# Kernel tuning notes

Measured on AMD Instinct MI355X. Metric: run time of the kernel, lower is better.

## Reference

```python
import jax, jax.numpy as jnp
import numpy as np

D_MODEL = 1024
NUM_HEADS = 16
D_K = D_MODEL // NUM_HEADS
BATCH = 4
SEQ = 2048


def setup_inputs() -> dict:
    key = jax.random.key(0)
    ks = jax.random.split(key, 12)
    s = 0.02
    inp = {
        "Q": jax.random.normal(ks[0], (BATCH, SEQ, D_MODEL), jnp.float32),
        "K": jax.random.normal(ks[1], (BATCH, SEQ, D_MODEL), jnp.float32),
        "V": jax.random.normal(ks[2], (BATCH, SEQ, D_MODEL), jnp.float32),
        "mask": jnp.tril(jnp.ones((SEQ, SEQ), jnp.int32)),  # causal: 0 = masked
        "Wq": jax.random.normal(ks[3], (D_MODEL, D_MODEL), jnp.float32) * s,
        "bq": jax.random.normal(ks[4], (D_MODEL,), jnp.float32) * s,
        "Wk": jax.random.normal(ks[5], (D_MODEL, D_MODEL), jnp.float32) * s,
        "bk": jax.random.normal(ks[6], (D_MODEL,), jnp.float32) * s,
        "Wv": jax.random.normal(ks[7], (D_MODEL, D_MODEL), jnp.float32) * s,
        "bv": jax.random.normal(ks[8], (D_MODEL,), jnp.float32) * s,
        "Wo": jax.random.normal(ks[9], (D_MODEL, D_MODEL), jnp.float32) * s,
        "bo": jax.random.normal(ks[10], (D_MODEL,), jnp.float32) * s,
    }
    return inp


def _split_heads(x):
    # (b, s, d_model) -> (b, h, s, d_k)
    b, s, _ = x.shape
    return x.reshape(b, s, NUM_HEADS, D_K).transpose(0, 2, 1, 3)


def reference(Q, K, V, mask, Wq, bq, Wk, bk, Wv, bv, Wo, bo):
    # Linear projections (torch Linear: x @ W^T + b)
    q = _split_heads(Q @ Wq.T + bq)  # (b, h, s, dk)
    k = _split_heads(K @ Wk.T + bk)
    v = _split_heads(V @ Wv.T + bv)
    scale = 1.0 / jnp.sqrt(jnp.asarray(D_K, q.dtype))
    scores = jnp.einsum("bhqd,bhkd->bhqk", q, k) * scale  # (b, h, s, s)
    scores = jnp.where(mask == 0, jnp.asarray(-jnp.inf, scores.dtype), scores)
    attn = jax.nn.softmax(scores, axis=-1)
    out = jnp.einsum("bhqk,bhkd->bhqd", attn, v)  # (b, h, s, dk)
    b, h, s, dk = out.shape
    out = out.transpose(0, 2, 1, 3).reshape(b, s, h * dk)  # combine heads
    return out @ Wo.T + bo
```

## Files before the change

### kernel.cpp

```cpp
#include <hip/hip_runtime.h>


typedef _Float16 f16;
typedef _Float16 f16x8 __attribute__((ext_vector_type(8)));
typedef _Float16 f16x4 __attribute__((ext_vector_type(4)));
typedef float floatx4 __attribute__((ext_vector_type(4)));
typedef float f32x16 __attribute__((ext_vector_type(16)));
typedef unsigned int uint4v __attribute__((ext_vector_type(4)));

#define SEQ 2048
#define DM 1024
#define NH 16
#define DK 64
#define MR 8192

#define QSCALE 0.18033688011112042f

#if __has_builtin(__builtin_amdgcn_exp2f)
#define EXP2(x) __builtin_amdgcn_exp2f(x)
#else
#define EXP2(x) __expf(0.6931471805599453f * (x))
#endif

__device__ __forceinline__ void gl_lds16(const void* g, void* lds) {
    __builtin_amdgcn_global_load_lds(
        (const __attribute__((address_space(1))) unsigned int*)g,
        (__attribute__((address_space(3))) unsigned int*)lds,
        16, 0, 0);
}

struct ConvArgs {
    const float* s[7];
    f16* d[7];
};

__global__ __launch_bounds__(256) void convk(ConvArgs a) {
    int bx = blockIdx.x;
    int t, base;
    if (bx < 3 * 8192) { t = bx / 8192; base = bx - t * 8192; }
    else { int r = bx - 3 * 8192; t = 3 + r / 1024; base = r - (t - 3) * 1024; }
    int i = base * 256 + threadIdx.x;
    float4 v = ((const float4*)a.s[t])[i];
    f16x4 o;
    o.x = (f16)v.x; o.y = (f16)v.y; o.z = (f16)v.z; o.w = (f16)v.w;
    ((f16x4*)a.d[t])[i] = o;
}

template <int MODE>
__device__ __forceinline__ void gemm_body(
    const f16* __restrict__ A, const f16* __restrict__ W,
    const float* __restrict__ bias, void* __restrict__ outp,
    int m0, int n0, float oscale, f16* As, f16* Bs)
{
    const int tid = threadIdx.x;
    const int wave = tid >> 6, lane = tid & 63;
    const int quad = lane >> 4, ln = lane & 15;
    const int wr = wave >> 1, wc = wave & 1;

    floatx4 acc[4][4] = {};

    for (int kt = 0; kt < 16; ++kt) {
        const int k0 = kt * 64;
#pragma unroll
        for (int s = 0; s < 4; ++s) {
            int c = s * 256 + tid;
            int row = c >> 3, lc = (c & 7) ^ (row & 7);
            gl_lds16(A + (size_t)(m0 + row) * 1024 + k0 + lc * 8,
                     (char*)As + (s * 256 + wave * 64) * 16);
        }
#pragma unroll
        for (int s = 0; s < 4; ++s) {
            int c = s * 256 + tid;
            int row = c >> 3, lc = (c & 7) ^ (row & 7);
            gl_lds16(W + (size_t)(n0 + row) * 1024 + k0 + lc * 8,
                     (char*)Bs + (s * 256 + wave * 64) * 16);
        }
        __syncthreads();
#pragma unroll
        for (int kk = 0; kk < 64; kk += 32) {
            const int cb = kk >> 3;
            f16x8 af[4], bf[4];
#pragma unroll
            for (int i = 0; i < 4; ++i) {
                int row = wr * 64 + i * 16 + ln;
                af[i] = *(const f16x8*)&As[row * 64 + (((cb + quad) ^ (ln & 7)) << 3)];
            }
#pragma unroll
            for (int j = 0; j < 4; ++j) {
                int row = wc * 64 + j * 16 + ln;
                bf[j] = *(const f16x8*)&Bs[row * 64 + (((cb + quad) ^ (ln & 7)) << 3)];
            }
#pragma unroll
            for (int i = 0; i < 4; ++i)
#pragma unroll
                for (int j = 0; j < 4; ++j)
                    acc[i][j] = __builtin_amdgcn_mfma_f32_16x16x32_f16(
                        af[i], bf[j], acc[i][j], 0, 0, 0);
        }
        __syncthreads();
    }

#pragma unroll
    for (int i = 0; i < 4; ++i) {
#pragma unroll
        for (int j = 0; j < 4; ++j) {
            int col = n0 + wc * 64 + j * 16 + ln;
            float bc = bias[col];
            int rowb = m0 + wr * 64 + i * 16 + quad * 4;
#pragma unroll
            for (int r = 0; r < 4; ++r) {
                float v = (acc[i][j][r] + bc) * oscale;
                int rm = rowb + r;
                if (MODE == 2) {
                    ((float*)outp)[(size_t)rm * 1024 + col] = v;
                } else {
                    int bb = rm >> 11, ss = rm & 2047;
                    int hh = col >> 6, dd = col & 63;
                    f16* o = (f16*)outp;
                    if (MODE == 0)
                        o[(((size_t)(bb * 16 + hh)) * 2048 + ss) * 64 + dd] = (f16)v;
                    else
                        o[(((size_t)(bb * 16 + hh)) * 64 + dd) * 2048 + ss] = (f16)v;
                }
            }
        }
    }
}

struct G3Args {
    const f16* A[3]; const f16* W[3]; const float* b[3]; f16* o[3];
};

__global__ __launch_bounds__(256, 2) void gemm_qkv(G3Args g) {
    __shared__ alignas(16) f16 As[128 * 64];
    __shared__ alignas(16) f16 Bs[128 * 64];
    const int z = blockIdx.z;
    const int m0 = blockIdx.x * 128, n0 = blockIdx.y * 128;
    if (z < 2)
        gemm_body<0>(g.A[z], g.W[z], g.b[z], g.o[z], m0, n0,
                     z == 0 ? QSCALE : 1.0f, As, Bs);
    else
        gemm_body<1>(g.A[2], g.W[2], g.b[2], g.o[2], m0, n0, 1.0f, As, Bs);
}

__global__ __launch_bounds__(256, 2) void gemm_out(
    const f16* __restrict__ A, const f16* __restrict__ W,
    const float* __restrict__ bias, float* __restrict__ outp)
{
    __shared__ alignas(16) f16 As[128 * 64];
    __shared__ alignas(16) f16 Bs[128 * 64];
    gemm_body<2>(A, W, bias, outp, blockIdx.x * 128, blockIdx.y * 128, 1.0f, As, Bs);
}

__global__ __launch_bounds__(256, 3) void attn_kernel(
    const f16* __restrict__ Qp, const f16* __restrict__ Kp,
    const f16* __restrict__ Vt, f16* __restrict__ Op)
{
    __shared__ alignas(16) f16 ks[128 * 64];
    __shared__ alignas(16) f16 vs[64 * 128];

    const int tid = threadIdx.x;
    const int wave = tid >> 6, lane = tid & 63;
    const int h = lane >> 5, c31 = lane & 31;
    const int bh = blockIdx.x;
    const f16* qb = Qp + (size_t)bh * SEQ * DK;
    const f16* kbp = Kp + (size_t)bh * SEQ * DK;
    const f16* vb = Vt + (size_t)bh * DK * SEQ;
    const int b = bh >> 4, hd = bh & 15;

    f16x8 ones;
#pragma unroll
    for (int e = 0; e < 8; ++e) ones[e] = (f16)1.0f;

    for (int half = 0; half < 2; ++half) {
        const int jt = half ? (15 - blockIdx.y) : blockIdx.y;
        const int q0 = jt * 128;

#pragma unroll
        for (int s = 0; s < 4; ++s) {
            int c = s * 256 + tid;
            int row = c >> 3, lc = (c & 7) ^ (row & 7);
            gl_lds16(qb + (size_t)(q0 + row) * 64 + lc * 8,
                     (char*)ks + (s * 256 + wave * 64) * 16);
        }
        __syncthreads();
        f16x8 bq[4];
#pragma unroll
        for (int t = 0; t < 4; ++t) {
            int row = wave * 32 + c31;
            bq[t] = *(const f16x8*)&ks[row * 64 + (((2 * t + h) ^ (row & 7)) << 3)];
        }
        __syncthreads();

        f32x16 oacc0 = {}, oacc1 = {}, lacc = {};

        const int nk = jt + 1;
        for (int kt = 0; kt < nk; ++kt) {
            const int k0 = kt * 128;
#pragma unroll
            for (int s = 0; s < 4; ++s) {
                int c = s * 256 + tid;
                int row = c >> 3, lc = (c & 7) ^ (row & 7);
                gl_lds16(kbp + (size_t)(k0 + row) * 64 + lc * 8,
                         (char*)ks + (s * 256 + wave * 64) * 16);
            }
#pragma unroll
            for (int s = 0; s < 4; ++s) {
                int c = s * 256 + tid;
                int row = c >> 4, lc = (c & 15) ^ (row & 15);
                gl_lds16(vb + (size_t)row * SEQ + k0 + lc * 8,
                         (char*)vs + (s * 256 + wave * 64) * 16);
            }
            __syncthreads();

            const bool diag = (kt == jt);
            const int qloc = wave * 32 + c31;

#pragma unroll
            for (int kb = 0; kb < 4; ++kb) {
                f32x16 sacc = {};
#pragma unroll
                for (int t = 0; t < 4; ++t) {
                    int row = kb * 32 + c31;
                    f16x8 ak = *(const f16x8*)&ks[row * 64 + (((2 * t + h) ^ (row & 7)) << 3)];
                    sacc = __builtin_amdgcn_mfma_f32_32x32x16_f16(
                        ak, bq[t], sacc, 0, 0, 0);
                }

                unsigned pg[4][2];
#pragma unroll
                for (int g = 0; g < 4; ++g) {
#pragma unroll
                    for (int j = 0; j < 2; ++j) {
                        const int r = 4 * g + 2 * j;
                        const int kg = kb * 32 + 8 * g + 4 * h + 2 * j;
                        float s0 = sacc[r], s1 = sacc[r + 1];
                        float p0 = (diag && kg > qloc) ? 0.0f : EXP2(s0);
                        float p1 = (diag && kg + 1 > qloc) ? 0.0f : EXP2(s1);
                        auto pp = __builtin_amdgcn_cvt_pkrtz(p0, p1);
                        pg[g][j] = __builtin_bit_cast(unsigned, pp);
                    }
                }

#pragma unroll
                for (int sub = 0; sub < 2; ++sub) {
                    const int s = 2 * kb + sub;
                    unsigned a0 = pg[2 * sub][0], a1 = pg[2 * sub][1];
                    unsigned b0 = pg[2 * sub + 1][0], b1 = pg[2 * sub + 1][1];
                    asm("v_permlane32_swap_b32 %0, %1" : "+v"(a0), "+v"(b0));
                    asm("v_permlane32_swap_b32 %0, %1" : "+v"(a1), "+v"(b1));
                    uint4v fw;
                    fw.x = a0; fw.y = a1; fw.z = b0; fw.w = b1;
                    f16x8 F = __builtin_bit_cast(f16x8, fw);

                    lacc = __builtin_amdgcn_mfma_f32_32x32x16_f16(
                        F, ones, lacc, 0, 0, 0);
                    {
                        int row = c31;
                        f16x8 bv = *(const f16x8*)&vs[row * 128 + (((2 * s + h) ^ (row & 15)) << 3)];
                        oacc0 = __builtin_amdgcn_mfma_f32_32x32x16_f16(
                            F, bv, oacc0, 0, 0, 0);
                    }
                    {
                        int row = 32 + c31;
                        f16x8 bv = *(const f16x8*)&vs[row * 128 + (((2 * s + h) ^ (row & 15)) << 3)];
                        oacc1 = __builtin_amdgcn_mfma_f32_32x32x16_f16(
                            F, bv, oacc1, 0, 0, 0);
                    }
                }
            }
            __syncthreads();
        }

#pragma unroll
        for (int r = 0; r < 16; ++r) {
            const int qr = (r & 3) + 8 * (r >> 2) + 4 * h;
            const int rowg = q0 + wave * 32 + qr;
            float inv = 1.0f / lacc[r];
            {
                int col = hd * 64 + c31;
                Op[((size_t)b * SEQ + rowg) * DM + col] = (f16)(oacc0[r] * inv);
            }
            {
                int col = hd * 64 + 32 + c31;
                Op[((size_t)b * SEQ + rowg) * DM + col] = (f16)(oacc1[r] * inv);
            }
        }
    }
}

extern "C" void kernel_launch(void* const* d_in, const int* in_sizes, int n_in,
                              void* d_out, int out_size, void* d_ws, size_t ws_size,
                              hipStream_t stream) {
    const float* Q  = (const float*)d_in[0];
    const float* K  = (const float*)d_in[1];
    const float* V  = (const float*)d_in[2];
    const float* Wq = (const float*)d_in[4];
    const float* bq = (const float*)d_in[5];
    const float* Wk = (const float*)d_in[6];
    const float* bk = (const float*)d_in[7];
    const float* Wv = (const float*)d_in[8];
    const float* bv = (const float*)d_in[9];
    const float* Wo = (const float*)d_in[10];
    const float* bo = (const float*)d_in[11];

    char* ws = (char*)d_ws;
    f16* Xq  = (f16*)(ws);
    f16* Xk  = Xq + (size_t)MR * DM;
    f16* Xv  = Xk + (size_t)MR * DM;
    f16* Wqb = Xv + (size_t)MR * DM;
    f16* Wkb = Wqb + (size_t)DM * DM;
    f16* Wvb = Wkb + (size_t)DM * DM;
    f16* Wob = Wvb + (size_t)DM * DM;
    f16* qp  = Wob + (size_t)DM * DM;
    f16* kp  = qp + (size_t)MR * DM;
    f16* vtp = kp + (size_t)MR * DM;

    ConvArgs ca;
    ca.s[0] = Q;  ca.d[0] = Xq;
    ca.s[1] = K;  ca.d[1] = Xk;
    ca.s[2] = V;  ca.d[2] = Xv;
    ca.s[3] = Wq; ca.d[3] = Wqb;
    ca.s[4] = Wk; ca.d[4] = Wkb;
    ca.s[5] = Wv; ca.d[5] = Wvb;
    ca.s[6] = Wo; ca.d[6] = Wob;
    convk<<<3 * 8192 + 4 * 1024, 256, 0, stream>>>(ca);

    G3Args g;
    g.A[0] = Xq; g.W[0] = Wqb; g.b[0] = bq; g.o[0] = qp;
    g.A[1] = Xk; g.W[1] = Wkb; g.b[1] = bk; g.o[1] = kp;
    g.A[2] = Xv; g.W[2] = Wvb; g.b[2] = bv; g.o[2] = vtp;
    gemm_qkv<<<dim3(64, 8, 3), 256, 0, stream>>>(g);

    attn_kernel<<<dim3(64, 8), 256, 0, stream>>>(qp, kp, vtp, Xq);

    gemm_out<<<dim3(64, 8), 256, 0, stream>>>(Xq, Wob, bo, (float*)d_out);
}
```

Baseline: 305.2 us.

## Double-buffer K/V tiles in attention kernel and specialize diagonal masking

The attention kernel now keeps two LDS buffers for K and V and issues the global-to-LDS loads for the next key tile while the current tile is computed, so load latency overlaps MFMA work. The causal mask check is moved into a template so only the diagonal tile pays for it. s_setprio hints are placed around the MFMA groups. LDS use doubles, so the launch bound drops from 3 to 2 blocks per CU, which reduces occupancy.

```diff
diff --git a/kernel.cpp b/kernel.cpp
--- a/kernel.cpp
+++ b/kernel.cpp
@@ -152,12 +152,99 @@
     gemm_body<2>(A, W, bias, outp, blockIdx.x * 128, blockIdx.y * 128, 1.0f, As, Bs);
 }
 
-__global__ __launch_bounds__(256, 3) void attn_kernel(
+__device__ __forceinline__ void stage_k(const f16* __restrict__ src, f16* buf,
+                                        int r0, int tid, int wave) {
+#pragma unroll
+    for (int s = 0; s < 4; ++s) {
+        int c = s * 256 + tid;
+        int row = c >> 3, lc = (c & 7) ^ (row & 7);
+        gl_lds16(src + (size_t)(r0 + row) * 64 + lc * 8,
+                 (char*)buf + (s * 256 + wave * 64) * 16);
+    }
+}
+
+__device__ __forceinline__ void stage_v(const f16* __restrict__ vb, f16* buf,
+                                        int k0, int tid, int wave) {
+#pragma unroll
+    for (int s = 0; s < 4; ++s) {
+        int c = s * 256 + tid;
+        int row = c >> 4, lc = (c & 15) ^ (row & 15);
+        gl_lds16(vb + (size_t)row * SEQ + k0 + lc * 8,
+                 (char*)buf + (s * 256 + wave * 64) * 16);
+    }
+}
+
+template <bool DIAG>
+__device__ __forceinline__ void attn_tile(
+    const f16* ksb, const f16* vsb, const f16x8 bq[4], const f16x8 ones,
+    f32x16& oacc0, f32x16& oacc1, f32x16& lacc, int h, int c31, int qloc)
+{
+#pragma unroll
+    for (int kb = 0; kb < 4; ++kb) {
+        f32x16 sacc = {};
+        __builtin_amdgcn_s_setprio(1);
+#pragma unroll
+        for (int t = 0; t < 4; ++t) {
+            int row = kb * 32 + c31;
+            f16x8 ak = *(const f16x8*)&ksb[row * 64 + (((2 * t + h) ^ (row & 7)) << 3)];
+            sacc = __builtin_amdgcn_mfma_f32_32x32x16_f16(ak, bq[t], sacc, 0, 0, 0);
+        }
+        __builtin_amdgcn_s_setprio(0);
+
+        unsigned pg[4][2];
+#pragma unroll
+        for (int g = 0; g < 4; ++g) {
+#pragma unroll
+            for (int j = 0; j < 2; ++j) {
+                const int r = 4 * g + 2 * j;
+                float p0, p1;
+                if (DIAG) {
+                    const int kg = kb * 32 + 8 * g + 4 * h + 2 * j;
+                    p0 = (kg > qloc) ? 0.0f : EXP2(sacc[r]);
+                    p1 = (kg + 1 > qloc) ? 0.0f : EXP2(sacc[r + 1]);
+                } else {
+                    p0 = EXP2(sacc[r]);
+                    p1 = EXP2(sacc[r + 1]);
+                }
+                auto pp = __builtin_amdgcn_cvt_pkrtz(p0, p1);
+                pg[g][j] = __builtin_bit_cast(unsigned, pp);
+            }
+        }
+
+#pragma unroll
+        for (int sub = 0; sub < 2; ++sub) {
+            const int s = 2 * kb + sub;
+            unsigned a0 = pg[2 * sub][0], a1 = pg[2 * sub][1];
+            unsigned b0 = pg[2 * sub + 1][0], b1 = pg[2 * sub + 1][1];
+            asm("v_permlane32_swap_b32 %0, %1" : "+v"(a0), "+v"(b0));
+            asm("v_permlane32_swap_b32 %0, %1" : "+v"(a1), "+v"(b1));
+            uint4v fw;
+            fw.x = a0; fw.y = a1; fw.z = b0; fw.w = b1;
+            f16x8 F = __builtin_bit_cast(f16x8, fw);
+
+            __builtin_amdgcn_s_setprio(1);
+            lacc = __builtin_amdgcn_mfma_f32_32x32x16_f16(F, ones, lacc, 0, 0, 0);
+            {
+                int row = c31;
+                f16x8 bv = *(const f16x8*)&vsb[row * 128 + (((2 * s + h) ^ (row & 15)) << 3)];
+                oacc0 = __builtin_amdgcn_mfma_f32_32x32x16_f16(F, bv, oacc0, 0, 0, 0);
+            }
+            {
+                int row = 32 + c31;
+                f16x8 bv = *(const f16x8*)&vsb[row * 128 + (((2 * s + h) ^ (row & 15)) << 3)];
+                oacc1 = __builtin_amdgcn_mfma_f32_32x32x16_f16(F, bv, oacc1, 0, 0, 0);
+            }
+            __builtin_amdgcn_s_setprio(0);
+        }
+    }
+}
+
+__global__ __launch_bounds__(256, 2) void attn_kernel(
     const f16* __restrict__ Qp, const f16* __restrict__ Kp,
     const f16* __restrict__ Vt, f16* __restrict__ Op)
 {
-    __shared__ alignas(16) f16 ks[128 * 64];
-    __shared__ alignas(16) f16 vs[64 * 128];
+    __shared__ alignas(16) f16 ks[2][128 * 64];
+    __shared__ alignas(16) f16 vs[2][64 * 128];
 
     const int tid = threadIdx.x;
     const int wave = tid >> 6, lane = tid & 63;
@@ -175,101 +262,37 @@
     for (int half = 0; half < 2; ++half) {
         const int jt = half ? (15 - blockIdx.y) : blockIdx.y;
         const int q0 = jt * 128;
-
-#pragma unroll
-        for (int s = 0; s < 4; ++s) {
-            int c = s * 256 + tid;
-            int row = c >> 3, lc = (c & 7) ^ (row & 7);
-            gl_lds16(qb + (size_t)(q0 + row) * 64 + lc * 8,
-                     (char*)ks + (s * 256 + wave * 64) * 16);
-        }
+        const int nk = jt + 1;
+        const int qloc = wave * 32 + c31;
+
+        stage_k(qb, ks[0], q0, tid, wave);
         __syncthreads();
         f16x8 bq[4];
 #pragma unroll
         for (int t = 0; t < 4; ++t) {
             int row = wave * 32 + c31;
-            bq[t] = *(const f16x8*)&ks[row * 64 + (((2 * t + h) ^ (row & 7)) << 3)];
-        }
+            bq[t] = *(const f16x8*)&ks[0][row * 64 + (((2 * t + h) ^ (row & 7)) << 3)];
+        }
+        stage_k(kbp, ks[1], 0, tid, wave);
+        stage_v(vb, vs[1], 0, tid, wave);
         __syncthreads();
 
         f32x16 oacc0 = {}, oacc1 = {}, lacc = {};
 
-        const int nk = jt + 1;
+        int cur = 1;
         for (int kt = 0; kt < nk; ++kt) {
-            const int k0 = kt * 128;
-#pragma unroll
-            for (int s = 0; s < 4; ++s) {
-                int c = s * 256 + tid;
-                int row = c >> 3, lc = (c & 7) ^ (row & 7);
-                gl_lds16(kbp + (size_t)(k0 + row) * 64 + lc * 8,
-                         (char*)ks + (s * 256 + wave * 64) * 16);
-            }
-#pragma unroll
-            for (int s = 0; s < 4; ++s) {
-                int c = s * 256 + tid;
-                int row = c >> 4, lc = (c & 15) ^ (row & 15);
-                gl_lds16(vb + (size_t)row * SEQ + k0 + lc * 8,
-                         (char*)vs + (s * 256 + wave * 64) * 16);
-            }
+            if (kt + 1 < nk) {
+                stage_k(kbp, ks[cur ^ 1], (kt + 1) * 128, tid, wave);
+                stage_v(vb, vs[cur ^ 1], (kt + 1) * 128, tid, wave);
+            }
+            if (kt == nk - 1)
+                attn_tile<true>(ks[cur], vs[cur], bq, ones,
+                                oacc0, oacc1, lacc, h, c31, qloc);
+            else
+                attn_tile<false>(ks[cur], vs[cur], bq, ones,
+                                 oacc0, oacc1, lacc, h, c31, qloc);
             __syncthreads();
-
-            const bool diag = (kt == jt);
-            const int qloc = wave * 32 + c31;
-
-#pragma unroll
-            for (int kb = 0; kb < 4; ++kb) {
-                f32x16 sacc = {};
-#pragma unroll
-                for (int t = 0; t < 4; ++t) {
-                    int row = kb * 32 + c31;
-                    f16x8 ak = *(const f16x8*)&ks[row * 64 + (((2 * t + h) ^ (row & 7)) << 3)];
-                    sacc = __builtin_amdgcn_mfma_f32_32x32x16_f16(
-                        ak, bq[t], sacc, 0, 0, 0);
-                }
-
-                unsigned pg[4][2];
-#pragma unroll
-                for (int g = 0; g < 4; ++g) {
-#pragma unroll
-                    for (int j = 0; j < 2; ++j) {
-                        const int r = 4 * g + 2 * j;
-                        const int kg = kb * 32 + 8 * g + 4 * h + 2 * j;
-                        float s0 = sacc[r], s1 = sacc[r + 1];
-                        float p0 = (diag && kg > qloc) ? 0.0f : EXP2(s0);
-                        float p1 = (diag && kg + 1 > qloc) ? 0.0f : EXP2(s1);
-                        auto pp = __builtin_amdgcn_cvt_pkrtz(p0, p1);
-                        pg[g][j] = __builtin_bit_cast(unsigned, pp);
-                    }
-                }
-
-#pragma unroll
-                for (int sub = 0; sub < 2; ++sub) {
-                    const int s = 2 * kb + sub;
-                    unsigned a0 = pg[2 * sub][0], a1 = pg[2 * sub][1];
-                    unsigned b0 = pg[2 * sub + 1][0], b1 = pg[2 * sub + 1][1];
-                    asm("v_permlane32_swap_b32 %0, %1" : "+v"(a0), "+v"(b0));
-                    asm("v_permlane32_swap_b32 %0, %1" : "+v"(a1), "+v"(b1));
-                    uint4v fw;
-                    fw.x = a0; fw.y = a1; fw.z = b0; fw.w = b1;
-                    f16x8 F = __builtin_bit_cast(f16x8, fw);
-
-                    lacc = __builtin_amdgcn_mfma_f32_32x32x16_f16(
-                        F, ones, lacc, 0, 0, 0);
-                    {
-                        int row = c31;
-                        f16x8 bv = *(const f16x8*)&vs[row * 128 + (((2 * s + h) ^ (row & 15)) << 3)];
-                        oacc0 = __builtin_amdgcn_mfma_f32_32x32x16_f16(
-                            F, bv, oacc0, 0, 0, 0);
-                    }
-                    {
-                        int row = 32 + c31;
-                        f16x8 bv = *(const f16x8*)&vs[row * 128 + (((2 * s + h) ^ (row & 15)) << 3)];
-                        oacc1 = __builtin_amdgcn_mfma_f32_32x32x16_f16(
-                            F, bv, oacc1, 0, 0, 0);
-                    }
-                }
-            }
-            __syncthreads();
+            cur ^= 1;
         }
 
 #pragma unroll
```

Measured after the change: 310.5 us. About the same (+1.8%).
